# Optimization experiments

Hardware: AMD Instinct MI355X
Metric: run time of the kernel (lower is better)

The kernel has to match this reference:

```python
import jax, jax.numpy as jnp
import numpy as np


def _conv(x, w, b, pad):
    # x: (BN, Cin, H, W), w: (Cout, Cin, kh, kw) -> (BN, Cout, H, W)
    y = jax.lax.conv_general_dilated(x, w, window_strides=(1, 1),
                                     padding=[(pad, pad), (pad, pad)],
                                     dimension_numbers=('NCHW', 'OIHW', 'NCHW'))
    return y + b[None, :, None, None]


def setup_inputs() -> dict:
    key = jax.random.key(0)
    ks = jax.random.split(key, 32)
    B, N, H, W = 1, 24, 60, 80
    COR = 4 * (2 * 3 + 1) ** 2 + 1  # 197
    f = jnp.float32

    def p(k, shape, scale=0.02):
        return (jax.random.normal(k, shape, dtype=f) * scale)

    return {
        'net':  jax.random.normal(ks[0], (B, N, 128, H, W), dtype=f),
        'inp':  jax.random.normal(ks[1], (B, N, 128, H, W), dtype=f),
        'corr': jax.random.normal(ks[2], (B, N, COR, H, W), dtype=f),
        'flow': jax.random.normal(ks[3], (B, N, 3, H, W), dtype=f),
        # corr encoder: 1x1 197->128, 3x3 128->128
        'w_ce1': p(ks[4], (128, COR, 1, 1)), 'b_ce1': jnp.zeros((128,), f),
        'w_ce2': p(ks[5], (128, 128, 3, 3)), 'b_ce2': jnp.zeros((128,), f),
        # flow encoder: 7x7 3->128, 3x3 128->64
        'w_fe1': p(ks[6], (128, 3, 7, 7)),   'b_fe1': jnp.zeros((128,), f),
        'w_fe2': p(ks[7], (64, 128, 3, 3)),  'b_fe2': jnp.zeros((64,), f),
        # ConvGRU gates: 3x3 (128 hidden + 320 input = 448) -> 128
        'w_z': p(ks[8], (128, 448, 3, 3)),   'b_z': jnp.zeros((128,), f),
        'w_r': p(ks[9], (128, 448, 3, 3)),   'b_r': jnp.zeros((128,), f),
        'w_q': p(ks[10], (128, 448, 3, 3)),  'b_q': jnp.zeros((128,), f),
        # delta head: 3x3 128->128, 3x3 128->3
        'w_d1': p(ks[11], (128, 128, 3, 3)), 'b_d1': jnp.zeros((128,), f),
        'w_d2': p(ks[12], (3, 128, 3, 3)),   'b_d2': jnp.zeros((3,), f),
        # weight head: 3x3 128->128, 3x3 128->3 (+sigmoid)
        'w_w1': p(ks[13], (128, 128, 3, 3)), 'b_w1': jnp.zeros((128,), f),
        'w_w2': p(ks[14], (3, 128, 3, 3)),   'b_w2': jnp.zeros((3,), f),
    }


def reference(net, inp, corr, flow,
              w_ce1, b_ce1, w_ce2, b_ce2,
              w_fe1, b_fe1, w_fe2, b_fe2,
              w_z, b_z, w_r, b_r, w_q, b_q,
              w_d1, b_d1, w_d2, b_d2,
              w_w1, b_w1, w_w2, b_w2):
    B, N, C, H, W = net.shape
    h = net.reshape(B * N, C, H, W)
    x_inp = inp.reshape(B * N, -1, H, W)
    c = corr.reshape(B * N, -1, H, W)
    fl = flow.reshape(B * N, -1, H, W)

    # correlation encoder
    c = jax.nn.relu(_conv(c, w_ce1, b_ce1, 0))
    c = jax.nn.relu(_conv(c, w_ce2, b_ce2, 1))
    # flow encoder
    fl = jax.nn.relu(_conv(fl, w_fe1, b_fe1, 3))
    fl = jax.nn.relu(_conv(fl, w_fe2, b_fe2, 1))

    # ConvGRU: inputs = cat(inp, corr_feat, flow_feat) -> 320 channels
    x = jnp.concatenate([x_inp, c, fl], axis=1)
    hx = jnp.concatenate([h, x], axis=1)  # 448 ch
    z = jax.nn.sigmoid(_conv(hx, w_z, b_z, 1))
    r = jax.nn.sigmoid(_conv(hx, w_r, b_r, 1))
    q = jnp.tanh(_conv(jnp.concatenate([r * h, x], axis=1), w_q, b_q, 1))
    h = (1.0 - z) * h + z * q

    # heads (GradientClip is identity in forward)
    delta = _conv(jax.nn.relu(_conv(h, w_d1, b_d1, 1)), w_d2, b_d2, 1)
    weight = jax.nn.sigmoid(_conv(jax.nn.relu(_conv(h, w_w1, b_w1, 1)), w_w2, b_w2, 1))

    delta = delta.reshape(B, N, 3, H, W).transpose(0, 1, 3, 4, 2)
    weight = weight.reshape(B, N, 3, H, W).transpose(0, 1, 3, 4, 2)
    net_out = h.reshape(B, N, -1, H, W)
    return (net_out, delta, weight)
```

## Files before the change

### kernel.cpp

```cpp
#include <hip/hip_runtime.h>
#include <stdint.h>
#include <string.h>

#define PXI 4800
#define BNI 24

typedef short bf16x8 __attribute__((ext_vector_type(8)));
typedef float f32x4 __attribute__((ext_vector_type(4)));

__device__ __forceinline__ uint16_t f2b(float f) {
  uint32_t u = __float_as_uint(f);
  u += 0x7fffu + ((u >> 16) & 1u);
  return (uint16_t)(u >> 16);
}
__device__ __forceinline__ float b2f(uint16_t b) {
  return __uint_as_float(((uint32_t)b) << 16);
}
__device__ __forceinline__ float sigm(float x) {
  return 1.0f / (1.0f + __expf(-x));
}

struct SrcDesc {
  const void* p;
  int nstride;
  int coff;
  int pixstride;
  int creal;
  int is_f32;
};

struct ConvParams {
  SrcDesc srcs[14];
  int KS, cog_total, ncb, mode;
  const uint16_t* wpk;
  const float* bias0;
  const float* bias1;
  uint16_t* out0; int ostride0, ochoff0;
  uint16_t* out1; int ostride1, ochoff1;
  const uint16_t* zbuf;
  const uint16_t* hbf;
  const float* netf32;
  float* houtf32;
};

template<int DSPAN, int CW>
__global__ __launch_bounds__(256, 2) void conv_mfma(ConvParams P) {
  constexpr int PAD = (DSPAN - 1) / 2;
  constexpr int NR = 2;
  constexpr int NRS = NR + DSPAN - 1;
  constexpr int UP = 80 + 2 * PAD;
  constexpr int UPITCH = 82 * 64;
  constexpr int NT = DSPAN * DSPAN;
  constexpr int CB = 4 * CW;
  __shared__ __align__(16) uint8_t smem[NRS * UPITCH];
  const int tid = threadIdx.x;
  const int wave = tid >> 6, lane = tid & 63;
  const int bx = blockIdx.x;
  const int total = gridDim.x;
  const int id = (bx & 7) * (total >> 3) + (bx >> 3);
  const int cbk = id % P.ncb;
  const int rg = id / P.ncb;
  const int n = rg / 30, y0 = (rg - n * 30) * NR;
  const int cog0 = cbk * CB + wave * CW;

  f32x4 acc[CW][NR][5];
#pragma unroll
  for (int c = 0; c < CW; ++c)
#pragma unroll
    for (int r = 0; r < NR; ++r)
#pragma unroll
      for (int t = 0; t < 5; ++t)
        acc[c][r][t] = f32x4{0.f, 0.f, 0.f, 0.f};

  const int pxl = lane & 15;
  const int hi16 = (lane >> 4) * 16;
  const int tapstride = P.cog_total * P.KS * 512;
  const uint16_t* wl = P.wpk + lane * 8;

  for (int ks = 0; ks < P.KS; ++ks) {
    __syncthreads();
    const SrcDesc d = P.srcs[ks];
    if (!d.is_f32) {
      const uint16_t* bp = (const uint16_t*)d.p + (size_t)n * d.nstride + d.coff;
      for (int c = tid; c < NRS * UP * 4; c += 256) {
        int rs = c / (UP * 4);
        int rem = c - rs * (UP * 4);
        int u = rem >> 2, kq = rem & 3;
        int ysrc = y0 + rs - PAD;
        int xs = u - PAD;
        uint4 v; v.x = 0; v.y = 0; v.z = 0; v.w = 0;
        if ((unsigned)ysrc < 60u && (unsigned)xs < 80u)
          v = *(const uint4*)(bp + (size_t)(ysrc * 80 + xs) * d.pixstride + kq * 8);
        *(uint4*)(smem + rs * UPITCH + ((u * 64 + kq * 16) ^ ((u & 7) << 4))) = v;
      }
    } else {
      const int ci = tid >> 3, xg = tid & 7;
      const bool cok = (d.coff + ci) < d.creal;
      const float* fp = (const float*)d.p + (size_t)n * d.nstride +
                        (size_t)(d.coff + ci) * PXI;
#pragma unroll
      for (int rs = 0; rs < NRS; ++rs) {
#pragma unroll
        for (int j = 0; j < 10; ++j) {
          int x = xg + j * 8;
          float v = cok ? fp[(y0 + rs) * 80 + x] : 0.f;
          *(uint16_t*)(smem + rs * UPITCH + ((x * 64 + ci * 2) ^ ((x & 7) << 4))) = f2b(v);
        }
      }
    }
    __syncthreads();
    const uint16_t* wk0 = wl + ((size_t)cog0 * P.KS + ks) * 512;
#pragma unroll 1
    for (int tap = 0; tap < NT; ++tap) {
      bf16x8 a[CW];
#pragma unroll
      for (int c = 0; c < CW; ++c)
        a[c] = *(const bf16x8*)(wk0 + (size_t)tap * tapstride + (size_t)c * (P.KS * 512));
      const int dy = (DSPAN == 3) ? ((tap * 11) >> 5) : 0;
      const int dx = tap - dy * 3;
      const int u0 = pxl + dx;
      const uint8_t* brow = smem + dy * UPITCH + ((u0 * 64 + hi16) ^ ((u0 & 7) << 4));
#pragma unroll
      for (int r = 0; r < NR; ++r) {
#pragma unroll
        for (int t = 0; t < 5; ++t) {
          bf16x8 b = *(const bf16x8*)(brow + r * UPITCH + t * 1024);
#pragma unroll
          for (int c = 0; c < CW; ++c)
            acc[c][r][t] = __builtin_amdgcn_mfma_f32_16x16x32_bf16(a[c], b, acc[c][r][t], 0, 0, 0);
        }
      }
    }
  }

  const int rq = lane >> 4;
  for (int c = 0; c < CW; ++c) {
    const int co0 = (cog0 + c) * 16 + rq * 4;
    for (int r = 0; r < NR; ++r) {
      for (int t = 0; t < 5; ++t) {
        const int px = (y0 + r) * 80 + t * 16 + pxl;
        const size_t gpix = (size_t)n * PXI + px;
        float v[4];
#pragma unroll
        for (int rr = 0; rr < 4; ++rr) {
          int co = co0 + rr;
          float bia = (P.bias1 && co >= 128) ? P.bias1[co - 128] : P.bias0[co];
          v[rr] = acc[c][r][t][rr] + bia;
        }
        if (P.mode == 0) {
          uint16_t* op; int cb2;
          if (P.out1 && co0 >= 128) { op = P.out1 + gpix * (size_t)P.ostride1 + P.ochoff1; cb2 = co0 - 128; }
          else                      { op = P.out0 + gpix * (size_t)P.ostride0 + P.ochoff0; cb2 = co0; }
          uint64_t w = 0;
#pragma unroll
          for (int rr = 0; rr < 4; ++rr)
            w |= (uint64_t)f2b(fmaxf(v[rr], 0.f)) << (16 * rr);
          *(uint64_t*)(op + cb2) = w;
        } else if (P.mode == 1) {
          if (co0 < 128) {
            uint64_t w = 0;
#pragma unroll
            for (int rr = 0; rr < 4; ++rr)
              w |= (uint64_t)f2b(sigm(v[rr])) << (16 * rr);
            *(uint64_t*)(P.out0 + gpix * 128 + co0) = w;
          } else {
            uint64_t hw = *(const uint64_t*)(P.hbf + gpix * 448 + (co0 - 128));
            uint64_t w = 0;
#pragma unroll
            for (int rr = 0; rr < 4; ++rr) {
              float rgt = sigm(v[rr]);
              float h = b2f((uint16_t)(hw >> (16 * rr)));
              w |= (uint64_t)f2b(rgt * h) << (16 * rr);
            }
            *(uint64_t*)(P.out1 + gpix * 128 + (co0 - 128)) = w;
          }
        } else {
          uint64_t zw = *(const uint64_t*)(P.zbuf + gpix * 128 + co0);
          uint64_t w = 0;
#pragma unroll
          for (int rr = 0; rr < 4; ++rr) {
            float qv = tanhf(v[rr]);
            float z = b2f((uint16_t)(zw >> (16 * rr)));
            size_t hidx = ((size_t)n * 128 + co0 + rr) * PXI + px;
            float h = P.netf32[hidx];
            float hn = (1.f - z) * h + z * qv;
            P.houtf32[hidx] = hn;
            w |= (uint64_t)f2b(hn) << (16 * rr);
          }
          *(uint64_t*)(P.out0 + gpix * 128 + co0) = w;
        }
      }
    }
  }
}

__global__ __launch_bounds__(256) void nchw2nhwc(const float* src, uint16_t* dst,
                                                 int C, int pixstride, int choff) {
  const int n = blockIdx.y;
  const int px = blockIdx.x * 256 + threadIdx.x;
  if (px >= PXI) return;
  const float* sp = src + (size_t)n * C * PXI + px;
  uint16_t* dp = dst + ((size_t)n * PXI + px) * pixstride + choff;
  for (int c = 0; c < C; c += 8) {
    uint32_t pk[4];
#pragma unroll
    for (int j = 0; j < 4; ++j) {
      uint32_t lo = f2b(sp[(size_t)(c + 2 * j) * PXI]);
      uint32_t hi = f2b(sp[(size_t)(c + 2 * j + 1) * PXI]);
      pk[j] = lo | (hi << 16);
    }
    uint4 v; v.x = pk[0]; v.y = pk[1]; v.z = pk[2]; v.w = pk[3];
    *(uint4*)(dp + c) = v;
  }
}

__global__ __launch_bounds__(256) void im2col_fe1(const float* flow, uint16_t* F2col) {
  __shared__ float tile[3 * 7 * 88];
  __shared__ uint32_t lut[160];
  const int y = blockIdx.x, n = blockIdx.y;
  const int tid = threadIdx.x;
  if (tid < 160) {
    int k = tid;
    if (k < 147) {
      int ci = k / 49, rem = k - ci * 49;
      int ky = rem / 7, kx = rem - ky * 7;
      lut[k] = (uint32_t)ci | ((uint32_t)ky << 8) | ((uint32_t)kx << 16);
    } else lut[k] = 0xFFFFFFFFu;
  }
  for (int c = tid; c < 3 * 7 * 86; c += 256) {
    int ci = c / 602, rem = c - ci * 602;
    int ky = rem / 86, xi = rem - ky * 86;
    int ysrc = y + ky - 3, x = xi - 3;
    float v = 0.f;
    if ((unsigned)ysrc < 60u && (unsigned)x < 80u)
      v = flow[((size_t)(n * 3 + ci) * 60 + ysrc) * 80 + x];
    tile[(ci * 7 + ky) * 88 + xi] = v;
  }
  __syncthreads();
  uint16_t* op = F2col + ((size_t)n * PXI + y * 80) * 160;
  for (int c = tid; c < 80 * 20; c += 256) {
    int px = c / 20, q = c - px * 20;
    int k0 = q * 8;
    uint32_t pk[4];
#pragma unroll
    for (int j = 0; j < 4; ++j) {
      uint16_t w0 = 0, w1 = 0;
      uint32_t l0 = lut[k0 + 2 * j], l1 = lut[k0 + 2 * j + 1];
      if (l0 != 0xFFFFFFFFu)
        w0 = f2b(tile[((l0 & 0xFF) * 7 + ((l0 >> 8) & 0xFF)) * 88 + px + (l0 >> 16)]);
      if (l1 != 0xFFFFFFFFu)
        w1 = f2b(tile[((l1 & 0xFF) * 7 + ((l1 >> 8) & 0xFF)) * 88 + px + (l1 >> 16)]);
      pk[j] = (uint32_t)w0 | ((uint32_t)w1 << 16);
    }
    uint4 v; v.x = pk[0]; v.y = pk[1]; v.z = pk[2]; v.w = pk[3];
    *(uint4*)(op + (size_t)px * 160 + k0) = v;
  }
}

__global__ __launch_bounds__(256) void pack_w(const float* w, uint16_t* wpk,
    int Cout, int Cin, int taps, int CPAD, int cobase, int cogTotal) {
  int idx = blockIdx.x * 256 + threadIdx.x;
  int total = Cout * CPAD * taps;
  if (idx >= total) return;
  int ci = idx % CPAD;
  int rest = idx / CPAD;
  int co = rest % Cout;
  int tap = rest / Cout;
  float v = (ci < Cin) ? w[((size_t)co * Cin + ci) * taps + tap] : 0.f;
  int cog = (cobase + co) >> 4;
  int ks = ci >> 5;
  int lane = ((cobase + co) & 15) | (((ci >> 3) & 3) << 4);
  int KS = CPAD >> 5;
  size_t off = ((size_t)(tap * cogTotal + cog) * KS + ks) * 512 + lane * 8 + (ci & 7);
  wpk[off] = f2b(v);
}

__global__ __launch_bounds__(256) void dw2_kernel(const uint16_t* D1, const uint16_t* W1,
    const float* wd, const float* wwt, const float* bd, const float* bw,
    float* out_delta, float* out_weight) {
  __shared__ float wl[2 * 9 * 3 * 128];
  const int tid = threadIdx.x;
  for (int c = tid; c < 6912; c += 256) {
    int s = c / 3456, rem = c - s * 3456;
    int j = rem / 1152, rem2 = rem - j * 1152;
    int ci = rem2 / 9, tap = rem2 - ci * 9;
    const float* src = s ? wwt : wd;
    wl[((s * 9 + tap) * 3 + j) * 128 + ci] = src[rem];
  }
  __syncthreads();
  int gid = blockIdx.x * 256 + tid;
  if (gid >= BNI * PXI) return;
  int n = gid / PXI, px = gid - n * PXI;
  int y = px / 80, x = px - y * 80;
  float accd[3] = {bd[0], bd[1], bd[2]};
  float accw[3] = {bw[0], bw[1], bw[2]};
  for (int tap = 0; tap < 9; ++tap) {
    int dy = tap / 3, dxm = tap - dy * 3;
    int ys = y + dy - 1, xs = x + dxm - 1;
    if ((unsigned)ys >= 60u || (unsigned)xs >= 80u) continue;
    const uint16_t* dp = D1 + ((size_t)n * PXI + ys * 80 + xs) * 128;
    const uint16_t* wp = W1 + ((size_t)n * PXI + ys * 80 + xs) * 128;
    const float* wtd = &wl[(0 * 9 + tap) * 3 * 128];
    const float* wtw = &wl[(9 + tap) * 3 * 128];
    for (int cq = 0; cq < 16; ++cq) {
      uint4 dv4 = *(const uint4*)(dp + cq * 8);
      uint4 wv4 = *(const uint4*)(wp + cq * 8);
      float dv[8], wv[8];
      const uint32_t* du = (const uint32_t*)&dv4;
      const uint32_t* wu = (const uint32_t*)&wv4;
#pragma unroll
      for (int e = 0; e < 4; ++e) {
        dv[2 * e] = b2f((uint16_t)du[e]); dv[2 * e + 1] = b2f((uint16_t)(du[e] >> 16));
        wv[2 * e] = b2f((uint16_t)wu[e]); wv[2 * e + 1] = b2f((uint16_t)(wu[e] >> 16));
      }
#pragma unroll
      for (int j = 0; j < 3; ++j) {
        f32x4 wa = *(const f32x4*)(wtd + j * 128 + cq * 8);
        f32x4 wb = *(const f32x4*)(wtd + j * 128 + cq * 8 + 4);
        f32x4 va = *(const f32x4*)(wtw + j * 128 + cq * 8);
        f32x4 vb = *(const f32x4*)(wtw + j * 128 + cq * 8 + 4);
#pragma unroll
        for (int e = 0; e < 4; ++e) {
          accd[j] += dv[e] * wa[e] + dv[e + 4] * wb[e];
          accw[j] += wv[e] * va[e] + wv[e + 4] * vb[e];
        }
      }
    }
  }
  size_t ob = ((size_t)n * PXI + px) * 3;
#pragma unroll
  for (int j = 0; j < 3; ++j) {
    out_delta[ob + j] = accd[j];
    out_weight[ob + j] = sigm(accw[j]);
  }
}

extern "C" void kernel_launch(void* const* d_in, const int* in_sizes, int n_in,
                              void* d_out, int out_size, void* d_ws, size_t ws_size,
                              hipStream_t stream) {
  (void)in_sizes; (void)n_in; (void)out_size; (void)ws_size;
  const float* net  = (const float*)d_in[0];
  const float* inp  = (const float*)d_in[1];
  const float* corr = (const float*)d_in[2];
  const float* flow = (const float*)d_in[3];
  const float* w_ce1 = (const float*)d_in[4];   const float* b_ce1 = (const float*)d_in[5];
  const float* w_ce2 = (const float*)d_in[6];   const float* b_ce2 = (const float*)d_in[7];
  const float* w_fe1 = (const float*)d_in[8];   const float* b_fe1 = (const float*)d_in[9];
  const float* w_fe2 = (const float*)d_in[10];  const float* b_fe2 = (const float*)d_in[11];
  const float* w_z  = (const float*)d_in[12];   const float* b_z  = (const float*)d_in[13];
  const float* w_r  = (const float*)d_in[14];   const float* b_r  = (const float*)d_in[15];
  const float* w_q  = (const float*)d_in[16];   const float* b_q  = (const float*)d_in[17];
  const float* w_d1 = (const float*)d_in[18];   const float* b_d1 = (const float*)d_in[19];
  const float* w_d2 = (const float*)d_in[20];   const float* b_d2 = (const float*)d_in[21];
  const float* w_w1 = (const float*)d_in[22];   const float* b_w1 = (const float*)d_in[23];
  const float* w_w2 = (const float*)d_in[24];   const float* b_w2 = (const float*)d_in[25];

  uint8_t* ws = (uint8_t*)d_ws;
  size_t off = 0;
  auto alloc = [&](size_t b) { size_t o = off; off += (b + 255) & ~(size_t)255; return o; };
  uint16_t* wpk_ce1 = (uint16_t*)(ws + alloc(57344));
  uint16_t* wpk_ce2 = (uint16_t*)(ws + alloc(294912));
  uint16_t* wpk_fe1 = (uint16_t*)(ws + alloc(40960));
  uint16_t* wpk_fe2 = (uint16_t*)(ws + alloc(147456));
  uint16_t* wpk_zr  = (uint16_t*)(ws + alloc(2064384));
  uint16_t* wpk_q   = (uint16_t*)(ws + alloc(1032192));
  uint16_t* wpk_dw  = (uint16_t*)(ws + alloc(589824));
  uint16_t* X448 = (uint16_t*)(ws + alloc((size_t)BNI * PXI * 448 * 2));
  uint16_t* C1   = (uint16_t*)(ws + alloc((size_t)BNI * PXI * 128 * 2));
  uint16_t* F1   = (uint16_t*)(ws + alloc((size_t)BNI * PXI * 128 * 2));
  uint16_t* Zb   = (uint16_t*)(ws + alloc((size_t)BNI * PXI * 128 * 2));
  uint16_t* RHb  = (uint16_t*)(ws + alloc((size_t)BNI * PXI * 128 * 2));
  uint16_t* F2col = Zb;

  auto packs = [&](const float* w, uint16_t* dst, int Cout, int Cin, int taps,
                   int CPAD, int cobase, int cogT) {
    int total = Cout * CPAD * taps;
    pack_w<<<(total + 255) / 256, 256, 0, stream>>>(w, dst, Cout, Cin, taps, CPAD, cobase, cogT);
  };
  packs(w_ce1, wpk_ce1, 128, 197, 1, 224, 0, 8);
  packs(w_ce2, wpk_ce2, 128, 128, 9, 128, 0, 8);
  packs(w_fe1, wpk_fe1, 128, 147, 1, 160, 0, 8);
  packs(w_fe2, wpk_fe2, 64, 128, 9, 128, 0, 4);
  packs(w_z,  wpk_zr, 128, 448, 9, 448, 0, 16);
  packs(w_r,  wpk_zr, 128, 448, 9, 448, 128, 16);
  packs(w_q,  wpk_q,  128, 448, 9, 448, 0, 8);
  packs(w_d1, wpk_dw, 128, 128, 9, 128, 0, 16);
  packs(w_w1, wpk_dw, 128, 128, 9, 128, 128, 16);

  nchw2nhwc<<<dim3(19, BNI), 256, 0, stream>>>(net, X448, 128, 448, 0);
  nchw2nhwc<<<dim3(19, BNI), 256, 0, stream>>>(inp, X448, 128, 448, 128);
  im2col_fe1<<<dim3(60, BNI), 256, 0, stream>>>(flow, F2col);

  const int GR = BNI * 30;
  ConvParams p;
  memset(&p, 0, sizeof(p));
  for (int ks = 0; ks < 5; ++ks) p.srcs[ks] = SrcDesc{F2col, PXI * 160, ks * 32, 160, 0, 0};
  p.KS = 5; p.cog_total = 8; p.ncb = 1; p.mode = 0;
  p.wpk = wpk_fe1; p.bias0 = b_fe1;
  p.out0 = F1; p.ostride0 = 128; p.ochoff0 = 0;
  conv_mfma<1, 2><<<GR, 256, 0, stream>>>(p);
  memset(&p, 0, sizeof(p));
  for (int ks = 0; ks < 7; ++ks) p.srcs[ks] = SrcDesc{corr, 197 * PXI, ks * 32, 0, 197, 1};
  p.KS = 7; p.cog_total = 8; p.ncb = 1; p.mode = 0;
  p.wpk = wpk_ce1; p.bias0 = b_ce1;
  p.out0 = C1; p.ostride0 = 128; p.ochoff0 = 0;
  conv_mfma<1, 2><<<GR, 256, 0, stream>>>(p);
  memset(&p, 0, sizeof(p));
  for (int ks = 0; ks < 4; ++ks) p.srcs[ks] = SrcDesc{C1, PXI * 128, ks * 32, 128, 0, 0};
  p.KS = 4; p.cog_total = 8; p.ncb = 1; p.mode = 0;
  p.wpk = wpk_ce2; p.bias0 = b_ce2;
  p.out0 = X448; p.ostride0 = 448; p.ochoff0 = 256;
  conv_mfma<3, 2><<<GR, 256, 0, stream>>>(p);
  memset(&p, 0, sizeof(p));
  for (int ks = 0; ks < 4; ++ks) p.srcs[ks] = SrcDesc{F1, PXI * 128, ks * 32, 128, 0, 0};
  p.KS = 4; p.cog_total = 4; p.ncb = 1; p.mode = 0;
  p.wpk = wpk_fe2; p.bias0 = b_fe2;
  p.out0 = X448; p.ostride0 = 448; p.ochoff0 = 384;
  conv_mfma<3, 1><<<GR, 256, 0, stream>>>(p);
  memset(&p, 0, sizeof(p));
  for (int ks = 0; ks < 14; ++ks) p.srcs[ks] = SrcDesc{X448, PXI * 448, ks * 32, 448, 0, 0};
  p.KS = 14; p.cog_total = 16; p.ncb = 2; p.mode = 1;
  p.wpk = wpk_zr; p.bias0 = b_z; p.bias1 = b_r;
  p.out0 = Zb; p.out1 = RHb; p.hbf = X448;
  conv_mfma<3, 2><<<GR * 2, 256, 0, stream>>>(p);
  memset(&p, 0, sizeof(p));
  for (int ks = 0; ks < 4; ++ks)  p.srcs[ks] = SrcDesc{RHb, PXI * 128, ks * 32, 128, 0, 0};
  for (int ks = 4; ks < 14; ++ks) p.srcs[ks] = SrcDesc{X448, PXI * 448, 128 + (ks - 4) * 32, 448, 0, 0};
  p.KS = 14; p.cog_total = 8; p.ncb = 1; p.mode = 2;
  p.wpk = wpk_q; p.bias0 = b_q;
  p.out0 = C1; p.zbuf = Zb; p.netf32 = net; p.houtf32 = (float*)d_out;
  conv_mfma<3, 2><<<GR, 256, 0, stream>>>(p);
  memset(&p, 0, sizeof(p));
  for (int ks = 0; ks < 4; ++ks) p.srcs[ks] = SrcDesc{C1, PXI * 128, ks * 32, 128, 0, 0};
  p.KS = 4; p.cog_total = 16; p.ncb = 2; p.mode = 0;
  p.wpk = wpk_dw; p.bias0 = b_d1; p.bias1 = b_w1;
  p.out0 = Zb; p.ostride0 = 128; p.ochoff0 = 0;
  p.out1 = RHb; p.ostride1 = 128; p.ochoff1 = 0;
  conv_mfma<3, 2><<<GR * 2, 256, 0, stream>>>(p);
  float* dout = (float*)d_out;
  dw2_kernel<<<450, 256, 0, stream>>>(Zb, RHb, w_d2, w_w2, b_d2, b_w2,
                                      dout + 14745600, dout + 15091200);
}
```

Measured before the change: 1.065 ms.

## Remap waves to 2x2 row-by-channel tiles covering all output channels per block

Each block now computes every output channel for its two-row strip. The four waves form a 2x2 grid: two halves of the output channels by two rows, each wave holding a CWW-wide channel slice for one row. Previously the z/r and head convs split channels across two blocks, and each block staged the same input rows into shared memory. Removing that split halves the input staging and global reads for those convs. The cost is more accumulator registers per wave at CWW=8 (40 f32x4), which may cause spilling or lower occupancy, and half as many blocks for the 256-channel convs.

```diff
diff --git a/kernel.cpp b/kernel.cpp
--- a/kernel.cpp
+++ b/kernel.cpp
@@ -31,7 +31,7 @@
 
 struct ConvParams {
   SrcDesc srcs[14];
-  int KS, cog_total, ncb, mode;
+  int KS, cog_total, mode;
   const uint16_t* wpk;
   const float* bias0;
   const float* bias1;
@@ -43,38 +43,34 @@
   float* houtf32;
 };
 
-template<int DSPAN, int CW>
+template<int DSPAN, int CWW>
 __global__ __launch_bounds__(256, 2) void conv_mfma(ConvParams P) {
   constexpr int PAD = (DSPAN - 1) / 2;
-  constexpr int NR = 2;
-  constexpr int NRS = NR + DSPAN - 1;
+  constexpr int NRB = 2;
+  constexpr int NRS = NRB + DSPAN - 1;
   constexpr int UP = 80 + 2 * PAD;
   constexpr int UPITCH = 82 * 64;
   constexpr int NT = DSPAN * DSPAN;
-  constexpr int CB = 4 * CW;
   __shared__ __align__(16) uint8_t smem[NRS * UPITCH];
   const int tid = threadIdx.x;
   const int wave = tid >> 6, lane = tid & 63;
+  const int cw = wave & 1, rw = wave >> 1;
   const int bx = blockIdx.x;
-  const int total = gridDim.x;
-  const int id = (bx & 7) * (total >> 3) + (bx >> 3);
-  const int cbk = id % P.ncb;
-  const int rg = id / P.ncb;
-  const int n = rg / 30, y0 = (rg - n * 30) * NR;
-  const int cog0 = cbk * CB + wave * CW;
-
-  f32x4 acc[CW][NR][5];
-#pragma unroll
-  for (int c = 0; c < CW; ++c)
-#pragma unroll
-    for (int r = 0; r < NR; ++r)
-#pragma unroll
-      for (int t = 0; t < 5; ++t)
-        acc[c][r][t] = f32x4{0.f, 0.f, 0.f, 0.f};
+  const int rg = (bx & 7) * (gridDim.x >> 3) + (bx >> 3);
+  const int n = rg / 30, y0 = (rg - n * 30) * NRB;
+  const int cog0 = cw * CWW;
+
+  f32x4 acc[CWW][5];
+#pragma unroll
+  for (int c = 0; c < CWW; ++c)
+#pragma unroll
+    for (int t = 0; t < 5; ++t)
+      acc[c][t] = f32x4{0.f, 0.f, 0.f, 0.f};
 
   const int pxl = lane & 15;
   const int hi16 = (lane >> 4) * 16;
-  const int tapstride = P.cog_total * P.KS * 512;
+  const int kstride = P.KS * 512;
+  const int tapstride = P.cog_total * kstride;
   const uint16_t* wl = P.wpk + lane * 8;
 
   for (int ks = 0; ks < P.KS; ++ks) {
@@ -112,83 +108,78 @@
     const uint16_t* wk0 = wl + ((size_t)cog0 * P.KS + ks) * 512;
 #pragma unroll 1
     for (int tap = 0; tap < NT; ++tap) {
-      bf16x8 a[CW];
-#pragma unroll
-      for (int c = 0; c < CW; ++c)
-        a[c] = *(const bf16x8*)(wk0 + (size_t)tap * tapstride + (size_t)c * (P.KS * 512));
+      bf16x8 a[CWW];
+#pragma unroll
+      for (int c = 0; c < CWW; ++c)
+        a[c] = *(const bf16x8*)(wk0 + (size_t)tap * tapstride + (size_t)c * kstride);
       const int dy = (DSPAN == 3) ? ((tap * 11) >> 5) : 0;
       const int dx = tap - dy * 3;
       const int u0 = pxl + dx;
-      const uint8_t* brow = smem + dy * UPITCH + ((u0 * 64 + hi16) ^ ((u0 & 7) << 4));
-#pragma unroll
-      for (int r = 0; r < NR; ++r) {
-#pragma unroll
-        for (int t = 0; t < 5; ++t) {
-          bf16x8 b = *(const bf16x8*)(brow + r * UPITCH + t * 1024);
-#pragma unroll
-          for (int c = 0; c < CW; ++c)
-            acc[c][r][t] = __builtin_amdgcn_mfma_f32_16x16x32_bf16(a[c], b, acc[c][r][t], 0, 0, 0);
+      const uint8_t* brow = smem + (rw + dy) * UPITCH + ((u0 * 64 + hi16) ^ ((u0 & 7) << 4));
+#pragma unroll
+      for (int t = 0; t < 5; ++t) {
+        bf16x8 b = *(const bf16x8*)(brow + t * 1024);
+#pragma unroll
+        for (int c = 0; c < CWW; ++c)
+          acc[c][t] = __builtin_amdgcn_mfma_f32_16x16x32_bf16(a[c], b, acc[c][t], 0, 0, 0);
+      }
+    }
+  }
+
+  const int rq = lane >> 4;
+  for (int c = 0; c < CWW; ++c) {
+    const int co0 = (cog0 + c) * 16 + rq * 4;
+    for (int t = 0; t < 5; ++t) {
+      const int px = (y0 + rw) * 80 + t * 16 + pxl;
+      const size_t gpix = (size_t)n * PXI + px;
+      float v[4];
+#pragma unroll
+      for (int rr = 0; rr < 4; ++rr) {
+        int co = co0 + rr;
+        float bia = (P.bias1 && co >= 128) ? P.bias1[co - 128] : P.bias0[co];
+        v[rr] = acc[c][t][rr] + bia;
+      }
+      if (P.mode == 0) {
+        uint16_t* op; int cb2;
+        if (P.out1 && co0 >= 128) { op = P.out1 + gpix * (size_t)P.ostride1 + P.ochoff1; cb2 = co0 - 128; }
+        else                      { op = P.out0 + gpix * (size_t)P.ostride0 + P.ochoff0; cb2 = co0; }
+        uint64_t w = 0;
+#pragma unroll
+        for (int rr = 0; rr < 4; ++rr)
+          w |= (uint64_t)f2b(fmaxf(v[rr], 0.f)) << (16 * rr);
+        *(uint64_t*)(op + cb2) = w;
+      } else if (P.mode == 1) {
+        if (co0 < 128) {
+          uint64_t w = 0;
+#pragma unroll
+          for (int rr = 0; rr < 4; ++rr)
+            w |= (uint64_t)f2b(sigm(v[rr])) << (16 * rr);
+          *(uint64_t*)(P.out0 + gpix * 128 + co0) = w;
+        } else {
+          uint64_t hw = *(const uint64_t*)(P.hbf + gpix * 448 + (co0 - 128));
+          uint64_t w = 0;
+#pragma unroll
+          for (int rr = 0; rr < 4; ++rr) {
+            float rgt = sigm(v[rr]);
+            float h = b2f((uint16_t)(hw >> (16 * rr)));
+            w |= (uint64_t)f2b(rgt * h) << (16 * rr);
+          }
+          *(uint64_t*)(P.out1 + gpix * 128 + (co0 - 128)) = w;
         }
-      }
-    }
-  }
-
-  const int rq = lane >> 4;
-  for (int c = 0; c < CW; ++c) {
-    const int co0 = (cog0 + c) * 16 + rq * 4;
-    for (int r = 0; r < NR; ++r) {
-      for (int t = 0; t < 5; ++t) {
-        const int px = (y0 + r) * 80 + t * 16 + pxl;
-        const size_t gpix = (size_t)n * PXI + px;
-        float v[4];
+      } else {
+        uint64_t zw = *(const uint64_t*)(P.zbuf + gpix * 128 + co0);
+        uint64_t w = 0;
 #pragma unroll
         for (int rr = 0; rr < 4; ++rr) {
-          int co = co0 + rr;
-          float bia = (P.bias1 && co >= 128) ? P.bias1[co - 128] : P.bias0[co];
-          v[rr] = acc[c][r][t][rr] + bia;
+          float qv = tanhf(v[rr]);
+          float z = b2f((uint16_t)(zw >> (16 * rr)));
+          size_t hidx = ((size_t)n * 128 + co0 + rr) * PXI + px;
+          float h = P.netf32[hidx];
+          float hn = (1.f - z) * h + z * qv;
+          P.houtf32[hidx] = hn;
+          w |= (uint64_t)f2b(hn) << (16 * rr);
         }
-        if (P.mode == 0) {
-          uint16_t* op; int cb2;
-          if (P.out1 && co0 >= 128) { op = P.out1 + gpix * (size_t)P.ostride1 + P.ochoff1; cb2 = co0 - 128; }
-          else                      { op = P.out0 + gpix * (size_t)P.ostride0 + P.ochoff0; cb2 = co0; }
-          uint64_t w = 0;
-#pragma unroll
-          for (int rr = 0; rr < 4; ++rr)
-            w |= (uint64_t)f2b(fmaxf(v[rr], 0.f)) << (16 * rr);
-          *(uint64_t*)(op + cb2) = w;
-        } else if (P.mode == 1) {
-          if (co0 < 128) {
-            uint64_t w = 0;
-#pragma unroll
-            for (int rr = 0; rr < 4; ++rr)
-              w |= (uint64_t)f2b(sigm(v[rr])) << (16 * rr);
-            *(uint64_t*)(P.out0 + gpix * 128 + co0) = w;
-          } else {
-            uint64_t hw = *(const uint64_t*)(P.hbf + gpix * 448 + (co0 - 128));
-            uint64_t w = 0;
-#pragma unroll
-            for (int rr = 0; rr < 4; ++rr) {
-              float rgt = sigm(v[rr]);
-              float h = b2f((uint16_t)(hw >> (16 * rr)));
-              w |= (uint64_t)f2b(rgt * h) << (16 * rr);
-            }
-            *(uint64_t*)(P.out1 + gpix * 128 + (co0 - 128)) = w;
-          }
-        } else {
-          uint64_t zw = *(const uint64_t*)(P.zbuf + gpix * 128 + co0);
-          uint64_t w = 0;
-#pragma unroll
-          for (int rr = 0; rr < 4; ++rr) {
-            float qv = tanhf(v[rr]);
-            float z = b2f((uint16_t)(zw >> (16 * rr)));
-            size_t hidx = ((size_t)n * 128 + co0 + rr) * PXI + px;
-            float h = P.netf32[hidx];
-            float hn = (1.f - z) * h + z * qv;
-            P.houtf32[hidx] = hn;
-            w |= (uint64_t)f2b(hn) << (16 * rr);
-          }
-          *(uint64_t*)(P.out0 + gpix * 128 + co0) = w;
-        }
+        *(uint64_t*)(P.out0 + gpix * 128 + co0) = w;
       }
     }
   }
@@ -395,48 +386,48 @@
   ConvParams p;
   memset(&p, 0, sizeof(p));
   for (int ks = 0; ks < 5; ++ks) p.srcs[ks] = SrcDesc{F2col, PXI * 160, ks * 32, 160, 0, 0};
-  p.KS = 5; p.cog_total = 8; p.ncb = 1; p.mode = 0;
+  p.KS = 5; p.cog_total = 8; p.mode = 0;
   p.wpk = wpk_fe1; p.bias0 = b_fe1;
   p.out0 = F1; p.ostride0 = 128; p.ochoff0 = 0;
-  conv_mfma<1, 2><<<GR, 256, 0, stream>>>(p);
+  conv_mfma<1, 4><<<GR, 256, 0, stream>>>(p);
   memset(&p, 0, sizeof(p));
   for (int ks = 0; ks < 7; ++ks) p.srcs[ks] = SrcDesc{corr, 197 * PXI, ks * 32, 0, 197, 1};
-  p.KS = 7; p.cog_total = 8; p.ncb = 1; p.mode = 0;
+  p.KS = 7; p.cog_total = 8; p.mode = 0;
   p.wpk = wpk_ce1; p.bias0 = b_ce1;
   p.out0 = C1; p.ostride0 = 128; p.ochoff0 = 0;
-  conv_mfma<1, 2><<<GR, 256, 0, stream>>>(p);
+  conv_mfma<1, 4><<<GR, 256, 0, stream>>>(p);
   memset(&p, 0, sizeof(p));
   for (int ks = 0; ks < 4; ++ks) p.srcs[ks] = SrcDesc{C1, PXI * 128, ks * 32, 128, 0, 0};
-  p.KS = 4; p.cog_total = 8; p.ncb = 1; p.mode = 0;
+  p.KS = 4; p.cog_total = 8; p.mode = 0;
   p.wpk = wpk_ce2; p.bias0 = b_ce2;
   p.out0 = X448; p.ostride0 = 448; p.ochoff0 = 256;
-  conv_mfma<3, 2><<<GR, 256, 0, stream>>>(p);
+  conv_mfma<3, 4><<<GR, 256, 0, stream>>>(p);
   memset(&p, 0, sizeof(p));
   for (int ks = 0; ks < 4; ++ks) p.srcs[ks] = SrcDesc{F1, PXI * 128, ks * 32, 128, 0, 0};
-  p.KS = 4; p.cog_total = 4; p.ncb = 1; p.mode = 0;
+  p.KS = 4; p.cog_total = 4; p.mode = 0;
   p.wpk = wpk_fe2; p.bias0 = b_fe2;
   p.out0 = X448; p.ostride0 = 448; p.ochoff0 = 384;
-  conv_mfma<3, 1><<<GR, 256, 0, stream>>>(p);
+  conv_mfma<3, 2><<<GR, 256, 0, stream>>>(p);
   memset(&p, 0, sizeof(p));
   for (int ks = 0; ks < 14; ++ks) p.srcs[ks] = SrcDesc{X448, PXI * 448, ks * 32, 448, 0, 0};
-  p.KS = 14; p.cog_total = 16; p.ncb = 2; p.mode = 1;
+  p.KS = 14; p.cog_total = 16; p.mode = 1;
   p.wpk = wpk_zr; p.bias0 = b_z; p.bias1 = b_r;
   p.out0 = Zb; p.out1 = RHb; p.hbf = X448;
-  conv_mfma<3, 2><<<GR * 2, 256, 0, stream>>>(p);
+  conv_mfma<3, 8><<<GR, 256, 0, stream>>>(p);
   memset(&p, 0, sizeof(p));
   for (int ks = 0; ks < 4; ++ks)  p.srcs[ks] = SrcDesc{RHb, PXI * 128, ks * 32, 128, 0, 0};
   for (int ks = 4; ks < 14; ++ks) p.srcs[ks] = SrcDesc{X448, PXI * 448, 128 + (ks - 4) * 32, 448, 0, 0};
-  p.KS = 14; p.cog_total = 8; p.ncb = 1; p.mode = 2;
+  p.KS = 14; p.cog_total = 8; p.mode = 2;
   p.wpk = wpk_q; p.bias0 = b_q;
   p.out0 = C1; p.zbuf = Zb; p.netf32 = net; p.houtf32 = (float*)d_out;
-  conv_mfma<3, 2><<<GR, 256, 0, stream>>>(p);
+  conv_mfma<3, 4><<<GR, 256, 0, stream>>>(p);
   memset(&p, 0, sizeof(p));
   for (int ks = 0; ks < 4; ++ks) p.srcs[ks] = SrcDesc{C1, PXI * 128, ks * 32, 128, 0, 0};
-  p.KS = 4; p.cog_total = 16; p.ncb = 2; p.mode = 0;
+  p.KS = 4; p.cog_total = 16; p.mode = 0;
   p.wpk = wpk_dw; p.bias0 = b_d1; p.bias1 = b_w1;
   p.out0 = Zb; p.ostride0 = 128; p.ochoff0 = 0;
   p.out1 = RHb; p.ostride1 = 128; p.ochoff1 = 0;
-  conv_mfma<3, 2><<<GR * 2, 256, 0, stream>>>(p);
+  conv_mfma<3, 8><<<GR, 256, 0, stream>>>(p);
   float* dout = (float*)d_out;
   dw2_kernel<<<450, 256, 0, stream>>>(Zb, RHb, w_d2, w_w2, b_d2, b_w2,
                                       dout + 14745600, dout + 15091200);
```

After: 2.228 ms (median of 2 runs). 2.09x slower.
